# Kernel tuning notes

Measured on AMD Instinct MI355X. Metric: run time of the kernel, lower is better.

The kernel has to match this reference:

```python
import jax, jax.numpy as jnp
import numpy as np


def setup_inputs() -> dict:
    key = jax.random.key(0)
    ks = jax.random.split(key, 8)
    B, n_users, n_items, F = 4096, 20000, 10000, 64
    return {
        "user_idx": jax.random.randint(ks[0], (B,), 0, n_users),
        "item_idx": jax.random.randint(ks[1], (B,), 0, n_items),
        "interactions": jax.random.randint(ks[2], (n_users + 1, n_items + 1), 0, 2).astype(jnp.int32),
        "user_embed_w": jax.random.normal(ks[3], (n_users + 1, F), jnp.float32) * 0.01,
        "item_embed_w": jax.random.normal(ks[4], (n_items + 1, F), jnp.float32) * 0.01,
        "proj_u_w": jax.random.normal(ks[5], (F, n_items), jnp.float32) * 0.01,
        "proj_i_w": jax.random.normal(ks[6], (F, n_users), jnp.float32) * 0.01,
        "logit_w": jax.random.normal(ks[7], (1, F), jnp.float32) * 0.1,
        "logit_b": jnp.zeros((1,), jnp.float32),
    }


def _hist_proj(slice_int, mask_col, proj_w):
    # slice_int: (B, N) int rows; zero out the target column per-row, sum, project, scale
    B = slice_int.shape[0]
    s = slice_int.astype(jnp.float32)
    s = s.at[jnp.arange(B), mask_col].set(0.0)
    ssum = jnp.clip(jnp.sum(s, axis=1, keepdims=True), 1.0, None)  # (B,1)
    return (s @ proj_w.T) / jnp.sqrt(ssum)  # (B,F)


def reference(user_idx, item_idx, interactions, user_embed_w, item_embed_w,
              proj_u_w, proj_i_w, logit_w, logit_b):
    # history paths: gather rows, mask the (u,i) entry, sum-normalize, dense project
    user_hist = _hist_proj(interactions[user_idx, :-1], item_idx, proj_u_w)      # (B,F)
    item_hist = _hist_proj(interactions.T[item_idx, :-1], user_idx, proj_i_w)    # (B,F)
    rep_user = user_embed_w[user_idx] + user_hist
    rep_item = item_embed_w[item_idx] + item_hist
    pred_vector = rep_user * rep_item                                            # GMF
    logit = pred_vector @ logit_w.T + logit_b                                    # (B,1)
    return logit[:, 0]
```

## Files before the change

### kernel.cpp

```cpp
#include <hip/hip_runtime.h>
#include <hip/hip_bf16.h>
#include <stdint.h>

#define B    4096
#define NU   20000
#define NI   10000
#define RS   10001
#define XAS  320
#define XTS  640
#define NKI  625
#define NKU  313
#define SPI  32
#define SPU  16
#define KCH  20

typedef __attribute__((ext_vector_type(8))) short bf16x8;
typedef __attribute__((ext_vector_type(4))) float f32x4;

__global__ __launch_bounds__(256) void k_packall(const int* __restrict__ X,
                                                 uint32_t* __restrict__ Xall) {
  int lane = threadIdx.x & 63, wv = threadIdx.x >> 6;
  int u = blockIdx.x * 4 + wv;
  const uint32_t* row = (const uint32_t*)(X + (size_t)u * RS);
  uint32_t* dst = Xall + (size_t)u * XAS;
  int h = (4 - (u & 3)) & 3;
  if (lane < 7) dst[313 + lane] = 0;
  uint32_t mh = (uint32_t)__ballot(lane < h && row[lane] != 0);
  uint32_t carry = h ? (mh << (32 - h)) : 0u;
  for (int it = 0; it < 40; ++it) {
    int c0 = h + it * 256 + lane * 4;
    uint4 v;
    if (c0 + 3 < NI) {
      v = *(const uint4*)(row + c0);
    } else {
      uint32_t t0 = (c0     < NI) ? row[c0]     : 0u;
      uint32_t t1 = (c0 + 1 < NI) ? row[c0 + 1] : 0u;
      uint32_t t2 = (c0 + 2 < NI) ? row[c0 + 2] : 0u;
      uint32_t t3 = (c0 + 3 < NI) ? row[c0 + 3] : 0u;
      v = make_uint4(t0, t1, t2, t3);
    }
    uint32_t nib = (v.x ? 1u : 0u) | (v.y ? 2u : 0u) | (v.z ? 4u : 0u) | (v.w ? 8u : 0u);
    uint32_t acc = nib << ((lane & 7) * 4);
    acc |= __shfl_xor(acc, 1);
    acc |= __shfl_xor(acc, 2);
    acc |= __shfl_xor(acc, 4);
    uint32_t prev = __shfl_up(acc, 8);
    if (lane < 8) prev = carry;
    uint32_t nextcarry = __shfl(acc, 63);
    uint32_t outw = h ? ((acc << h) | (prev >> (32 - h))) : acc;
    int k = it * 8 + (lane >> 3);
    if ((lane & 7) == 0 && k < 313) dst[k] = outw;
    carry = nextcarry;
  }
}

__global__ __launch_bounds__(256) void k_bitT(const unsigned long long* __restrict__ Xall,
                                              uint32_t* __restrict__ XallT) {
  int lane = threadIdx.x & 63, wid = threadIdx.x >> 6;
  int w = blockIdx.x * 4 + wid;
  int band = blockIdx.y;
  if (w >= 157) return;
  unsigned long long g[8];
#pragma unroll
  for (int c = 0; c < 8; c++) {
    int u = (band * 8 + c) * 64 + lane;
    g[c] = (u < NU) ? Xall[(size_t)u * (XAS / 2) + w] : 0ULL;
  }
  union { unsigned long long o[8]; uint4 q[4]; } T;
#pragma unroll
  for (int c = 0; c < 8; c++) {
    unsigned long long mym = 0;
#pragma unroll
    for (int jj = 0; jj < 64; jj++) {
      unsigned long long m = __ballot((int)((g[c] >> jj) & 1ULL));
      if (lane == jj) mym = m;
    }
    T.o[c] = mym;
  }
  int j = w * 64 + lane;
  uint4* dst = (uint4*)(XallT + (size_t)j * XTS + band * 16);
#pragma unroll
  for (int q = 0; q < 4; q++) dst[q] = T.q[q];
}

__global__ __launch_bounds__(256) void k_prepW2(const float* __restrict__ pi,
    const float* __restrict__ pu, uint4* __restrict__ WfI, uint4* __restrict__ WfU) {
  __shared__ float tile[64][33];
  const float* src; uint4* wfrag; int NSRC, ks;
  if (blockIdx.x < NKI) { src = pi; wfrag = WfI; NSRC = NU; ks = blockIdx.x; }
  else                  { src = pu; wfrag = WfU; NSRC = NI; ks = blockIdx.x - NKI; }
  int tid = threadIdx.x;
  {
    int f = tid >> 2, part = tid & 3;
    int ubase = ks * 32 + part * 8;
    const float* sp = src + (size_t)f * NSRC;
#pragma unroll
    for (int q = 0; q < 8; q++) {
      int u = ubase + q;
      tile[f][part * 8 + q] = (u < NSRC) ? sp[u] : 0.f;
    }
  }
  __syncthreads();
  int l = tid & 63, t = tid >> 6;
  int g = l >> 4, f = t * 16 + (l & 15);
  int u0 = g * 8;
  uint32_t w[4];
#pragma unroll
  for (int p = 0; p < 4; p++) {
    __hip_bfloat16 blo = __float2bfloat16(tile[f][u0 + 2 * p]);
    __hip_bfloat16 bhi = __float2bfloat16(tile[f][u0 + 2 * p + 1]);
    w[p] = (uint32_t)*(uint16_t*)&blo | ((uint32_t)*(uint16_t*)&bhi << 16);
  }
  wfrag[(size_t)ks * 256 + tid] = make_uint4(w[0], w[1], w[2], w[3]);
}

__global__ __launch_bounds__(256) void k_mfma2(
    const uint32_t* __restrict__ XallT, const uint32_t* __restrict__ Xall,
    const uint4* __restrict__ WfI, const uint4* __restrict__ WfU,
    const int* __restrict__ item_idx, const int* __restrict__ user_idx,
    float* __restrict__ partFI, float* __restrict__ partFU) {
  int lane = threadIdx.x & 63, wid = threadIdx.x >> 6;
  const uint32_t* bits; const uint4* wf; float* pf; const int* idx;
  int bstride, nk, seg, pair;
  if (blockIdx.x < 1024) {
    pair = blockIdx.x & 31; seg = blockIdx.x >> 5;
    bits = XallT; bstride = XTS; wf = WfI; pf = partFI; idx = item_idx; nk = NKI;
  } else {
    int bx = blockIdx.x - 1024;
    pair = bx & 31; seg = bx >> 5;
    bits = Xall; bstride = XAS; wf = WfU; pf = partFU; idx = user_idx; nk = NKU;
  }
  int b0 = pair * 128 + wid * 32;
  int r0 = b0 + (lane & 15);
  int g = lane >> 4;
  int kbeg = seg * KCH, kend = min(nk, kbeg + KCH);
  const uint32_t* brow0 = bits + (size_t)idx[r0] * bstride;
  const uint32_t* brow1 = bits + (size_t)idx[r0 + 16] * bstride;
  f32x4 acc0[4] = {{0,0,0,0},{0,0,0,0},{0,0,0,0},{0,0,0,0}};
  f32x4 acc1[4] = {{0,0,0,0},{0,0,0,0},{0,0,0,0},{0,0,0,0}};
  for (int ks = kbeg; ks < kend; ++ks) {
    uint32_t by0 = (brow0[ks] >> (g * 8)) & 0xffu;
    uint32_t by1 = (brow1[ks] >> (g * 8)) & 0xffu;
    union { bf16x8 v; uint32_t u[4]; } A0, A1;
#pragma unroll
    for (int p = 0; p < 4; p++) {
      A0.u[p] = (((by0 >> (2 * p)) & 1u) ? 0x3F80u : 0u) |
                (((by0 >> (2 * p + 1)) & 1u) ? 0x3F800000u : 0u);
      A1.u[p] = (((by1 >> (2 * p)) & 1u) ? 0x3F80u : 0u) |
                (((by1 >> (2 * p + 1)) & 1u) ? 0x3F800000u : 0u);
    }
    const uint4* wp = wf + (size_t)ks * 256 + lane;
#pragma unroll
    for (int t = 0; t < 4; t++) {
      union { bf16x8 v; uint4 q; } Bf;
      Bf.q = wp[t * 64];
      acc0[t] = __builtin_amdgcn_mfma_f32_16x16x32_bf16(A0.v, Bf.v, acc0[t], 0, 0, 0);
      acc1[t] = __builtin_amdgcn_mfma_f32_16x16x32_bf16(A1.v, Bf.v, acc1[t], 0, 0, 0);
    }
  }
#pragma unroll
  for (int t = 0; t < 4; t++)
#pragma unroll
    for (int r = 0; r < 4; r++) {
      int b = b0 + (lane >> 4) * 4 + r;
      int f = t * 16 + (lane & 15);
      pf[((size_t)seg * B + b) * 64 + f] = acc0[t][r];
      pf[((size_t)seg * B + (b + 16)) * 64 + f] = acc1[t][r];
    }
}

__global__ __launch_bounds__(256) void k_final(
    const float* __restrict__ partFI, const float* __restrict__ partFU,
    const uint32_t* __restrict__ XallT, const uint32_t* __restrict__ Xall,
    const int* __restrict__ user_idx, const int* __restrict__ item_idx,
    const int* __restrict__ X, const float* __restrict__ pi, const float* __restrict__ pu,
    const float* __restrict__ uew, const float* __restrict__ iew,
    const float* __restrict__ lw, const float* __restrict__ lb,
    float* __restrict__ out) {
  int gid = blockIdx.x * 256 + threadIdx.x;
  int b = gid >> 6, f = gid & 63;
  int u = user_idx[b], it = item_idx[b];
  float ai = 0.f, au = 0.f;
  for (int s = 0; s < SPI; s++) ai += partFI[((size_t)s * B + b) * 64 + f];
  for (int s = 0; s < SPU; s++) au += partFU[((size_t)s * B + b) * 64 + f];
  const uint32_t* rowi = XallT + (size_t)it * XTS;
  const uint32_t* rowu = Xall + (size_t)u * XAS;
  int ci = 0, cu = 0;
  for (int d = f; d < NKI; d += 64) ci += __popc(rowi[d]);
  for (int d = f; d < NKU; d += 64) cu += __popc(rowu[d]);
  for (int off = 32; off; off >>= 1) {
    ci += __shfl_xor(ci, off);
    cu += __shfl_xor(cu, off);
  }
  int xc = X[(size_t)u * RS + it];
  if (xc) {
    ai -= pi[(size_t)f * NU + u];  ci -= 1;
    au -= pu[(size_t)f * NI + it]; cu -= 1;
  }
  float di = (float)ci; if (di < 1.f) di = 1.f;
  float du = (float)cu; if (du < 1.f) du = 1.f;
  float repi = iew[(size_t)it * 64 + f] + ai / sqrtf(di);
  float repu = uew[(size_t)u * 64 + f] + au / sqrtf(du);
  float v = repu * repi * lw[f];
  for (int off = 32; off; off >>= 1) v += __shfl_xor(v, off);
  if ((threadIdx.x & 63) == 0) out[b] = v + lb[0];
}

extern "C" void kernel_launch(void* const* d_in, const int* in_sizes, int n_in,
                              void* d_out, int out_size, void* d_ws, size_t ws_size,
                              hipStream_t stream) {
  const int*   user_idx = (const int*)d_in[0];
  const int*   item_idx = (const int*)d_in[1];
  const int*   X        = (const int*)d_in[2];
  const float* uew      = (const float*)d_in[3];
  const float* iew      = (const float*)d_in[4];
  const float* pu       = (const float*)d_in[5];
  const float* pi       = (const float*)d_in[6];
  const float* lw       = (const float*)d_in[7];
  const float* lb       = (const float*)d_in[8];
  float* out = (float*)d_out;

  char* wsb = (char*)d_ws;
  uint32_t* Xall   = (uint32_t*)(wsb + 0);
  uint32_t* XallT  = (uint32_t*)(wsb + 25600000);
  uint4*    WfI    = (uint4*)(wsb + 51322880);
  uint4*    WfU    = (uint4*)(wsb + 53882880);
  float*    partFI = (float*)(wsb + 55164928);
  float*    partFU = (float*)(wsb + 88719360);

  k_prepW2<<<NKI + NKU, 256, 0, stream>>>(pi, pu, WfI, WfU);
  k_packall<<<5000, 256, 0, stream>>>(X, Xall);
  k_bitT<<<dim3(40, 40), 256, 0, stream>>>((const unsigned long long*)Xall, XallT);
  k_mfma2<<<1536, 256, 0, stream>>>(XallT, Xall, WfI, WfU, item_idx, user_idx,
                                    partFI, partFU);
  k_final<<<1024, 256, 0, stream>>>(partFI, partFU, XallT, Xall,
                                    user_idx, item_idx, X, pi, pu, uew, iew, lw, lb, out);
}
```

Before: 332.0 us.

## Replace ballot-based bit transpose with shuffle butterfly transpose via shared memory

The bit-matrix transpose kernel used 64 wave ballots per 64x64 tile. It now stages tiles in shared memory and transposes them with a six-level masked shuffle-xor butterfly, and its grid now covers 160 64-bit words per row. The packing kernel also drops the per-row misaligned-head handling and reads the int rows with scalar loads instead of uint4 vector loads. Workspace offsets are shifted to fit the larger transposed buffer. The risks are extra shared-memory traffic and possibly less efficient global loads in the packing kernel.

```diff
diff --git a/kernel.cpp b/kernel.cpp
--- a/kernel.cpp
+++ b/kernel.cpp
@@ -21,66 +21,78 @@
                                                  uint32_t* __restrict__ Xall) {
   int lane = threadIdx.x & 63, wv = threadIdx.x >> 6;
   int u = blockIdx.x * 4 + wv;
-  const uint32_t* row = (const uint32_t*)(X + (size_t)u * RS);
+  const int* row = X + (size_t)u * RS;
   uint32_t* dst = Xall + (size_t)u * XAS;
-  int h = (4 - (u & 3)) & 3;
-  if (lane < 7) dst[313 + lane] = 0;
-  uint32_t mh = (uint32_t)__ballot(lane < h && row[lane] != 0);
-  uint32_t carry = h ? (mh << (32 - h)) : 0u;
+  if (lane < 7) dst[313 + lane] = 0u;
   for (int it = 0; it < 40; ++it) {
-    int c0 = h + it * 256 + lane * 4;
-    uint4 v;
-    if (c0 + 3 < NI) {
-      v = *(const uint4*)(row + c0);
+    int c0 = it * 256 + lane * 4;
+    int v0, v1, v2, v3;
+    if (it < 39) {
+      v0 = row[c0]; v1 = row[c0 + 1]; v2 = row[c0 + 2]; v3 = row[c0 + 3];
     } else {
-      uint32_t t0 = (c0     < NI) ? row[c0]     : 0u;
-      uint32_t t1 = (c0 + 1 < NI) ? row[c0 + 1] : 0u;
-      uint32_t t2 = (c0 + 2 < NI) ? row[c0 + 2] : 0u;
-      uint32_t t3 = (c0 + 3 < NI) ? row[c0 + 3] : 0u;
-      v = make_uint4(t0, t1, t2, t3);
-    }
-    uint32_t nib = (v.x ? 1u : 0u) | (v.y ? 2u : 0u) | (v.z ? 4u : 0u) | (v.w ? 8u : 0u);
+      v0 = (c0     < NI) ? row[c0]     : 0;
+      v1 = (c0 + 1 < NI) ? row[c0 + 1] : 0;
+      v2 = (c0 + 2 < NI) ? row[c0 + 2] : 0;
+      v3 = (c0 + 3 < NI) ? row[c0 + 3] : 0;
+    }
+    uint32_t nib = (v0 ? 1u : 0u) | (v1 ? 2u : 0u) | (v2 ? 4u : 0u) | (v3 ? 8u : 0u);
     uint32_t acc = nib << ((lane & 7) * 4);
     acc |= __shfl_xor(acc, 1);
     acc |= __shfl_xor(acc, 2);
     acc |= __shfl_xor(acc, 4);
-    uint32_t prev = __shfl_up(acc, 8);
-    if (lane < 8) prev = carry;
-    uint32_t nextcarry = __shfl(acc, 63);
-    uint32_t outw = h ? ((acc << h) | (prev >> (32 - h))) : acc;
     int k = it * 8 + (lane >> 3);
-    if ((lane & 7) == 0 && k < 313) dst[k] = outw;
-    carry = nextcarry;
-  }
-}
-
-__global__ __launch_bounds__(256) void k_bitT(const unsigned long long* __restrict__ Xall,
+    if ((lane & 7) == 0 && k < 313) dst[k] = acc;
+  }
+}
+
+__global__ __launch_bounds__(256) void k_bitT(const uint32_t* __restrict__ Xall,
                                               uint32_t* __restrict__ XallT) {
-  int lane = threadIdx.x & 63, wid = threadIdx.x >> 6;
-  int w = blockIdx.x * 4 + wid;
-  int band = blockIdx.y;
-  if (w >= 157) return;
-  unsigned long long g[8];
-#pragma unroll
-  for (int c = 0; c < 8; c++) {
-    int u = (band * 8 + c) * 64 + lane;
-    g[c] = (u < NU) ? Xall[(size_t)u * (XAS / 2) + w] : 0ULL;
-  }
-  union { unsigned long long o[8]; uint4 q[4]; } T;
-#pragma unroll
-  for (int c = 0; c < 8; c++) {
-    unsigned long long mym = 0;
-#pragma unroll
-    for (int jj = 0; jj < 64; jj++) {
-      unsigned long long m = __ballot((int)((g[c] >> jj) & 1ULL));
-      if (lane == jj) mym = m;
-    }
-    T.o[c] = mym;
-  }
-  int j = w * 64 + lane;
-  uint4* dst = (uint4*)(XallT + (size_t)j * XTS + band * 16);
-#pragma unroll
-  for (int q = 0; q < 4; q++) dst[q] = T.q[q];
+  __shared__ uint32_t ilo[512][9], ihi[512][9];
+  __shared__ uint32_t olo[512][9], ohi[512][9];
+  int t = threadIdx.x;
+  int lane = t & 63, wd = t >> 6;
+  int W0 = blockIdx.x * 8;
+  int u0 = blockIdx.y * 512;
+  int rr = t >> 3, w = t & 7;
+  const unsigned long long* Xq = (const unsigned long long*)Xall;
+  unsigned long long* Tq = (unsigned long long*)XallT;
+  for (int i = 0; i < 16; ++i) {
+    int r = rr + 32 * i;
+    int u = u0 + r;
+    unsigned long long v = (u < NU) ? Xq[(size_t)u * (XAS / 2) + W0 + w] : 0ULL;
+    ilo[r][w] = (uint32_t)v;
+    ihi[r][w] = (uint32_t)(v >> 32);
+  }
+  __syncthreads();
+  const unsigned long long ML[6] = {
+    0x5555555555555555ULL, 0x3333333333333333ULL, 0x0F0F0F0F0F0F0F0FULL,
+    0x00FF00FF00FF00FFULL, 0x0000FFFF0000FFFFULL, 0x00000000FFFFFFFFULL };
+  for (int i = 0; i < 16; ++i) {
+    int tile = wd * 16 + i;
+    int c = tile >> 3, W = tile & 7;
+    int rowi = c * 64 + lane;
+    unsigned long long x = ((unsigned long long)ihi[rowi][W] << 32) | ilo[rowi][W];
+#pragma unroll
+    for (int lv = 0; lv < 6; ++lv) {
+      int s = 1 << lv;
+      unsigned long long m = ML[lv];
+      uint32_t xl = (uint32_t)x, xh = (uint32_t)(x >> 32);
+      unsigned long long y = ((unsigned long long)__shfl_xor(xh, s) << 32) |
+                             (uint32_t)__shfl_xor(xl, s);
+      x = (lane & s) ? ((x & ~m) | ((y & ~m) >> s))
+                     : ((x & m) | ((y & m) << s));
+    }
+    int rowo = W * 64 + lane;
+    olo[rowo][c] = (uint32_t)x;
+    ohi[rowo][c] = (uint32_t)(x >> 32);
+  }
+  __syncthreads();
+  for (int i = 0; i < 16; ++i) {
+    int r = rr + 32 * i;
+    int j = W0 * 64 + r;
+    unsigned long long v = ((unsigned long long)ohi[r][w] << 32) | olo[r][w];
+    Tq[(size_t)j * (XTS / 2) + blockIdx.y * 8 + w] = v;
+  }
 }
 
 __global__ __launch_bounds__(256) void k_prepW2(const float* __restrict__ pi,
@@ -223,14 +235,14 @@
   char* wsb = (char*)d_ws;
   uint32_t* Xall   = (uint32_t*)(wsb + 0);
   uint32_t* XallT  = (uint32_t*)(wsb + 25600000);
-  uint4*    WfI    = (uint4*)(wsb + 51322880);
-  uint4*    WfU    = (uint4*)(wsb + 53882880);
-  float*    partFI = (float*)(wsb + 55164928);
-  float*    partFU = (float*)(wsb + 88719360);
+  uint4*    WfI    = (uint4*)(wsb + 51814400);
+  uint4*    WfU    = (uint4*)(wsb + 54374400);
+  float*    partFI = (float*)(wsb + 55656448);
+  float*    partFU = (float*)(wsb + 89210880);
 
   k_prepW2<<<NKI + NKU, 256, 0, stream>>>(pi, pu, WfI, WfU);
   k_packall<<<5000, 256, 0, stream>>>(X, Xall);
-  k_bitT<<<dim3(40, 40), 256, 0, stream>>>((const unsigned long long*)Xall, XallT);
+  k_bitT<<<dim3(20, 40), 256, 0, stream>>>(Xall, XallT);
   k_mfma2<<<1536, 256, 0, stream>>>(XallT, Xall, WfI, WfU, item_idx, user_idx,
                                     partFI, partFU);
   k_final<<<1024, 256, 0, stream>>>(partFI, partFU, XallT, Xall,
```

New measurement: 304.1 us. 1.09x faster.
